# Performance work log

Measured on AMD Instinct MI355X. Metric: run time of the kernel, lower is better.

Reference implementation:

```python
import jax, jax.numpy as jnp
import numpy as np

N_NODES = 100000


def setup_inputs() -> dict:
    key = jax.random.key(0)
    ks = jax.random.split(key, 8)
    N, E, D_IN, D_OUT = N_NODES, 1600000, 64, 64
    return {
        "emb_src": jax.random.normal(ks[0], (N, D_IN), dtype=jnp.float32),
        "emb_dst": jax.random.normal(ks[1], (N, D_IN), dtype=jnp.float32),
        "edge_weight": jax.random.uniform(ks[2], (E,), dtype=jnp.float32),
        "W": jax.random.normal(ks[3], (D_IN, D_OUT), dtype=jnp.float32) / np.sqrt(D_IN),
        "b": jnp.zeros((D_OUT,), dtype=jnp.float32),
        "src_idx": jax.random.randint(ks[4], (E,), 0, N),
        "dst_idx": jax.random.randint(ks[5], (E,), 0, N),
        "user_indices": jax.random.randint(ks[6], (N,), 0, 1000000),
        "labels": jax.random.randint(ks[7], (N,), 0, 2),
        "perm": jnp.arange(N),
    }


def reference(emb_src, emb_dst, edge_weight, W, b, src_idx, dst_idx, user_indices, labels, perm):
    # DGL update_all(u_mul_e('embedding','weight','m'), sum('m','ft')):
    # gather source embeddings, scale by edge weight, scatter-sum into dst.
    msgs = emb_src[src_idx] * edge_weight[:, None]            # [E, D]
    ft = jax.ops.segment_sum(msgs, dst_idx, num_segments=N_NODES)  # [N, D]
    # aggregate == 'SUM': self embedding + aggregated neighborhood
    h = emb_dst + ft                                          # [N, D]
    # per-row np.where(itemlist == dst_ID) matching -> permutation gather
    users = user_indices[perm]
    labs = labels[perm]
    # last layer: tanh(Linear(h)) (dropout p=0 is identity)
    item_embeddings = jnp.tanh(h @ W + b)                     # [N, D_OUT]
    return item_embeddings, users, labs
```

## Files before the change

### kernel.cpp

```cpp
#include <hip/hip_runtime.h>
#include <hip/hip_fp16.h>

#define D 64
#define NQ (D / 4)
#define NB 512
#define NPB 196
#define LOCAL_BITS 8
#define LOCAL_MASK 255
#define SCAN_W 512
#define CAP 4096
#define CAPB 3584

#define HACC_STRIDE 17
#define SMEM_BYTES (D * D * 4 + NPB * HACC_STRIDE * 16)

__device__ __forceinline__ float fast_tanh(float x) {
    float e = __expf(2.0f * x);
    return 1.0f - 2.0f / (e + 1.0f);
}

struct f8 { float4 a, b; };

__global__ __launch_bounds__(512) void init_cursor_kernel(int* __restrict__ cursor)
{
    int t = threadIdx.x;
    if (t < NB) cursor[t] = t * CAPB;
}

__global__ __launch_bounds__(1024) void front_kernel(
    const int* __restrict__ src_idx,
    const int* __restrict__ dst_idx,
    const float* __restrict__ edge_weight,
    int* __restrict__ cursor,
    int2* __restrict__ payload,
    const int* __restrict__ user_indices,
    const int* __restrict__ labels,
    const int* __restrict__ perm,
    const float* __restrict__ emb_src,
    __half* __restrict__ emb_h,
    float* __restrict__ users_out,
    float* __restrict__ labs_out,
    int n_edges, int chunk, int n_nodes)
{
    __shared__ int hist[NB];
    __shared__ int blockbase[NB];
    __shared__ int cur[NB];
    const int tid = threadIdx.x;
    int lo = blockIdx.x * chunk;
    int hi = min(n_edges, lo + chunk);

    for (int i = tid; i < NB; i += 1024) { hist[i] = 0; cur[i] = 0; }
    __syncthreads();
    for (int e = lo + tid; e < hi; e += 1024)
        atomicAdd(&hist[(unsigned)dst_idx[e] / NPB], 1);
    __syncthreads();
    for (int i = tid; i < NB; i += 1024) {
        int c = hist[i];
        blockbase[i] = c ? atomicAdd(&cursor[i], c) : 0;
    }
    __syncthreads();
    for (int e = lo + tid; e < hi; e += 1024) {
        int d = dst_idx[e];
        unsigned bkt = (unsigned)d / NPB;
        int pos = blockbase[bkt] + atomicAdd(&cur[bkt], 1);
        if (pos < (int)(bkt + 1) * CAPB)
            payload[pos] = make_int2((src_idx[e] << LOCAL_BITS) | (d - (int)bkt * NPB),
                                     __float_as_int(edge_weight[e]));
    }

    const int gstride = gridDim.x * blockDim.x;
    const int t0 = blockIdx.x * blockDim.x + tid;
    for (int i = t0; i < n_nodes; i += gstride) {
        int p = perm[i];
        users_out[i] = (float)user_indices[p];
        labs_out[i]  = (float)labels[p];
    }
    const int n_cvt = n_nodes * NQ;
    for (int i = t0; i < n_cvt; i += gstride) {
        float4 v = reinterpret_cast<const float4*>(emb_src)[i];
        __half2 a, b;
        a.x = __float2half_rn(v.x); a.y = __float2half_rn(v.y);
        b.x = __float2half_rn(v.z); b.y = __float2half_rn(v.w);
        uint2 u;
        u.x = *reinterpret_cast<unsigned*>(&a);
        u.y = *reinterpret_cast<unsigned*>(&b);
        reinterpret_cast<uint2*>(emb_h)[i] = u;
    }
}

template <bool USE_H, bool FIXED_BASE>
__global__ __launch_bounds__(1024, 8) void fused_gather_gemm_kernel(
    const float* __restrict__ emb_src,
    const __half* __restrict__ emb_h,
    const float* __restrict__ emb_dst,
    const float* __restrict__ Wmat,
    const float* __restrict__ bias,
    const int2* __restrict__ payload,
    const int* __restrict__ base_or_cursor,
    const int* __restrict__ counts,
    float* __restrict__ out,
    int n_nodes)
{
    __shared__ __align__(16) char smem[SMEM_BYTES];
    float*  Ws     = reinterpret_cast<float*>(smem);
    float4* Hacc   = reinterpret_cast<float4*>(smem + D * D * 4);
    int2*   sedges = reinterpret_cast<int2*>(smem + D * D * 4);
    int*    cnt    = reinterpret_cast<int*>(smem + D * D * 4 + CAP * 8);
    int*    scn    = cnt + 256;
    int*    cur    = scn + 256;

    const int tid = threadIdx.x;
    const int b   = blockIdx.x;
    int start, end;
    if constexpr (FIXED_BASE) {
        start = b * CAPB;
        end   = min(base_or_cursor[b], start + CAPB);
    } else {
        start = base_or_cursor[b];
        end   = start + counts[b];
    }

    const int g8 = tid >> 3;
    const int q8 = tid & 7;
    const float4* esrc = reinterpret_cast<const float4*>(emb_src);

    reinterpret_cast<float4*>(Ws)[tid] = reinterpret_cast<const float4*>(Wmat)[tid];

    auto load_row = [&](unsigned src) -> f8 {
        f8 r;
        if constexpr (USE_H) {
            uint4 u = *reinterpret_cast<const uint4*>(emb_h + ((size_t)src << 6) + (q8 << 3));
            union { uint2 w; __half2 h2[2]; } c0, c1;
            c0.w = make_uint2(u.x, u.y);
            c1.w = make_uint2(u.z, u.w);
            float2 f0 = __half22float2(c0.h2[0]);
            float2 f1 = __half22float2(c0.h2[1]);
            float2 f2 = __half22float2(c1.h2[0]);
            float2 f3 = __half22float2(c1.h2[1]);
            r.a = make_float4(f0.x, f0.y, f1.x, f1.y);
            r.b = make_float4(f2.x, f2.y, f3.x, f3.y);
        } else {
            const float4* p = esrc + (size_t)src * NQ + (q8 << 1);
            r.a = p[0];
            r.b = p[1];
        }
        return r;
    };

    float4 accA[2], accB[2];
    #pragma unroll
    for (int k = 0; k < 2; ++k) {
        accA[k] = make_float4(0.f, 0.f, 0.f, 0.f);
        accB[k] = make_float4(0.f, 0.f, 0.f, 0.f);
    }

    for (int cbase = start; cbase < end; cbase += CAP) {
        const int m = min(end - cbase, CAP);

        for (int i = tid; i < 256; i += 1024) { cnt[i] = 0; cur[i] = 0; }
        __syncthreads();

        int2 pe[4];
        #pragma unroll
        for (int j = 0; j < 4; ++j) {
            int i = cbase + tid + j * 1024;
            if (tid + j * 1024 < m) {
                pe[j] = payload[i];
                atomicAdd(&cnt[pe[j].x & LOCAL_MASK], 1);
            }
        }
        __syncthreads();

        if (tid < 256) scn[tid] = cnt[tid];
        __syncthreads();
        #pragma unroll
        for (int d = 1; d < 256; d <<= 1) {
            int x = 0;
            if (tid < 256 && tid >= d) x = scn[tid - d];
            __syncthreads();
            if (tid < 256) scn[tid] += x;
            __syncthreads();
        }
        if (tid < 256) scn[tid] -= cnt[tid];
        __syncthreads();

        #pragma unroll
        for (int j = 0; j < 4; ++j) {
            if (tid + j * 1024 < m) {
                int local = pe[j].x & LOCAL_MASK;
                int pos = scn[local] + atomicAdd(&cur[local], 1);
                sedges[pos] = pe[j];
            }
        }
        __syncthreads();

        #pragma unroll
        for (int k = 0; k < 2; ++k) {
            int n = g8 + 128 * k;
            if (n < NPB) {
                int mm = cnt[n];
                int bs = scn[n];
                float4 aA = accA[k], aB = accB[k];
                for (int j = 0; j < mm; j += 4) {
                    int lim = mm - 1;
                    int2 e0 = sedges[bs + j];
                    int2 e1 = sedges[bs + min(j + 1, lim)];
                    int2 e2 = sedges[bs + min(j + 2, lim)];
                    int2 e3 = sedges[bs + min(j + 3, lim)];
                    f8 v0 = load_row((unsigned)e0.x >> LOCAL_BITS);
                    f8 v1 = load_row((unsigned)e1.x >> LOCAL_BITS);
                    f8 v2 = load_row((unsigned)e2.x >> LOCAL_BITS);
                    f8 v3 = load_row((unsigned)e3.x >> LOCAL_BITS);
                    float w0 = __int_as_float(e0.y);
                    float w1 = (j + 1 < mm) ? __int_as_float(e1.y) : 0.f;
                    float w2 = (j + 2 < mm) ? __int_as_float(e2.y) : 0.f;
                    float w3 = (j + 3 < mm) ? __int_as_float(e3.y) : 0.f;
                    aA.x += v0.a.x * w0 + v1.a.x * w1 + v2.a.x * w2 + v3.a.x * w3;
                    aA.y += v0.a.y * w0 + v1.a.y * w1 + v2.a.y * w2 + v3.a.y * w3;
                    aA.z += v0.a.z * w0 + v1.a.z * w1 + v2.a.z * w2 + v3.a.z * w3;
                    aA.w += v0.a.w * w0 + v1.a.w * w1 + v2.a.w * w2 + v3.a.w * w3;
                    aB.x += v0.b.x * w0 + v1.b.x * w1 + v2.b.x * w2 + v3.b.x * w3;
                    aB.y += v0.b.y * w0 + v1.b.y * w1 + v2.b.y * w2 + v3.b.y * w3;
                    aB.z += v0.b.z * w0 + v1.b.z * w1 + v2.b.z * w2 + v3.b.z * w3;
                    aB.w += v0.b.w * w0 + v1.b.w * w1 + v2.b.w * w2 + v3.b.w * w3;
                }
                accA[k] = aA; accB[k] = aB;
            }
        }
        __syncthreads();
    }

    const int node0 = b * NPB;
    #pragma unroll
    for (int k = 0; k < 2; ++k) {
        int n = g8 + 128 * k;
        if (n < NPB) {
            int node = node0 + n;
            float4 d0 = make_float4(0.f, 0.f, 0.f, 0.f);
            float4 d1 = make_float4(0.f, 0.f, 0.f, 0.f);
            if (node < n_nodes) {
                const float4* ed = reinterpret_cast<const float4*>(emb_dst)
                                 + (size_t)node * NQ + (q8 << 1);
                d0 = ed[0]; d1 = ed[1];
            }
            float4 aA = accA[k], aB = accB[k];
            aA.x += d0.x; aA.y += d0.y; aA.z += d0.z; aA.w += d0.w;
            aB.x += d1.x; aB.y += d1.y; aB.z += d1.z; aB.w += d1.w;
            Hacc[n * HACC_STRIDE + (q8 << 1)]     = aA;
            Hacc[n * HACC_STRIDE + (q8 << 1) + 1] = aB;
        }
    }
    __syncthreads();

    const int g = tid >> 4;
    const int q = tid & 15;
    const float4* Ws4 = reinterpret_cast<const float4*>(Ws);
    float4 bv = reinterpret_cast<const float4*>(bias)[q];
    #pragma unroll
    for (int k = 0; k < 4; ++k) {
        int n = g + 64 * k;
        int node = node0 + n;
        if (n < NPB && node < n_nodes) {
            float4 a = make_float4(0.f, 0.f, 0.f, 0.f);
            #pragma unroll 4
            for (int kk = 0; kk < 16; ++kk) {
                float4 hv = Hacc[n * HACC_STRIDE + kk];
                float4 w0 = Ws4[(4 * kk + 0) * 16 + q];
                float4 w1 = Ws4[(4 * kk + 1) * 16 + q];
                float4 w2 = Ws4[(4 * kk + 2) * 16 + q];
                float4 w3 = Ws4[(4 * kk + 3) * 16 + q];
                a.x += hv.x * w0.x + hv.y * w1.x + hv.z * w2.x + hv.w * w3.x;
                a.y += hv.x * w0.y + hv.y * w1.y + hv.z * w2.y + hv.w * w3.y;
                a.z += hv.x * w0.z + hv.y * w1.z + hv.z * w2.z + hv.w * w3.z;
                a.w += hv.x * w0.w + hv.y * w1.w + hv.z * w2.w + hv.w * w3.w;
            }
            float4 o;
            o.x = fast_tanh(a.x + bv.x);
            o.y = fast_tanh(a.y + bv.y);
            o.z = fast_tanh(a.z + bv.z);
            o.w = fast_tanh(a.w + bv.w);
            reinterpret_cast<float4*>(out)[(size_t)node * NQ + q] = o;
        }
    }
}

__global__ __launch_bounds__(256) void meta_kernel(
    const int* __restrict__ user_indices,
    const int* __restrict__ labels,
    const int* __restrict__ perm,
    const float* __restrict__ emb_src,
    __half* __restrict__ emb_h,
    float* __restrict__ users_out,
    float* __restrict__ labs_out,
    int* __restrict__ counts,
    int n_zero,
    int n_nodes)
{
    const int stride = gridDim.x * blockDim.x;
    int t0 = blockIdx.x * blockDim.x + threadIdx.x;
    if (counts)
        for (int i = t0; i < n_zero; i += stride) counts[i] = 0;
    for (int i = t0; i < n_nodes; i += stride) {
        int p = perm[i];
        users_out[i] = (float)user_indices[p];
        labs_out[i]  = (float)labels[p];
    }
    if (emb_h) {
        const int n_cvt = n_nodes * NQ;
        for (int i = t0; i < n_cvt; i += stride) {
            float4 v = reinterpret_cast<const float4*>(emb_src)[i];
            __half2 a, b;
            a.x = __float2half_rn(v.x); a.y = __float2half_rn(v.y);
            b.x = __float2half_rn(v.z); b.y = __float2half_rn(v.w);
            uint2 u;
            u.x = *reinterpret_cast<unsigned*>(&a);
            u.y = *reinterpret_cast<unsigned*>(&b);
            reinterpret_cast<uint2*>(emb_h)[i] = u;
        }
    }
}

__global__ __launch_bounds__(1024) void hist_bucket_kernel(
    const int* __restrict__ dst_idx,
    int* __restrict__ counts,
    int n_edges, int chunk)
{
    __shared__ int hist[NB];
    for (int i = threadIdx.x; i < NB; i += 1024) hist[i] = 0;
    __syncthreads();
    int lo = blockIdx.x * chunk;
    int hi = min(n_edges, lo + chunk);
    for (int e = lo + threadIdx.x; e < hi; e += 1024)
        atomicAdd(&hist[(unsigned)dst_idx[e] / NPB], 1);
    __syncthreads();
    for (int i = threadIdx.x; i < NB; i += 1024)
        if (hist[i]) atomicAdd(&counts[i], hist[i]);
}

__global__ __launch_bounds__(SCAN_W) void scan_small_kernel(
    const int* __restrict__ counts,
    int* __restrict__ base,
    int* __restrict__ cursor,
    int nb)
{
    __shared__ int s[SCAN_W];
    int t = threadIdx.x;
    int v = (t < nb) ? counts[t] : 0;
    s[t] = v;
    __syncthreads();
    #pragma unroll
    for (int d = 1; d < SCAN_W; d <<= 1) {
        int x = (t >= d) ? s[t - d] : 0;
        __syncthreads();
        s[t] += x;
        __syncthreads();
    }
    if (t < nb) { base[t] = s[t] - v; cursor[t] = s[t] - v; }
}

__global__ __launch_bounds__(1024) void scatter_bucket_kernel(
    const int* __restrict__ src_idx,
    const int* __restrict__ dst_idx,
    const float* __restrict__ edge_weight,
    int* __restrict__ cursor,
    int2* __restrict__ payload,
    int n_edges, int chunk)
{
    __shared__ int hist[NB];
    __shared__ int blockbase[NB];
    __shared__ int cur[NB];
    const int tid = threadIdx.x;
    int lo = blockIdx.x * chunk;
    int hi = min(n_edges, lo + chunk);

    for (int i = tid; i < NB; i += 1024) { hist[i] = 0; cur[i] = 0; }
    __syncthreads();
    for (int e = lo + tid; e < hi; e += 1024)
        atomicAdd(&hist[(unsigned)dst_idx[e] / NPB], 1);
    __syncthreads();
    for (int i = tid; i < NB; i += 1024) {
        int c = hist[i];
        blockbase[i] = c ? atomicAdd(&cursor[i], c) : 0;
    }
    __syncthreads();
    for (int e = lo + tid; e < hi; e += 1024) {
        int d = dst_idx[e];
        unsigned bkt = (unsigned)d / NPB;
        int pos = blockbase[bkt] + atomicAdd(&cur[bkt], 1);
        payload[pos] = make_int2((src_idx[e] << LOCAL_BITS) | (d - (int)bkt * NPB),
                                 __float_as_int(edge_weight[e]));
    }
}

__global__ __launch_bounds__(256) void init_h_kernel(
    const float* __restrict__ emb_dst, float* __restrict__ h, int n_nodes)
{
    const int stride = gridDim.x * blockDim.x;
    const int total4 = n_nodes * NQ;
    for (int i = blockIdx.x * blockDim.x + threadIdx.x; i < total4; i += stride)
        reinterpret_cast<float4*>(h)[i] = reinterpret_cast<const float4*>(emb_dst)[i];
}

__global__ __launch_bounds__(256) void scatter_kernel(
    const float* __restrict__ emb_src,
    const float* __restrict__ edge_weight,
    const int* __restrict__ src_idx,
    const int* __restrict__ dst_idx,
    float* __restrict__ h,
    int n_edges)
{
    int t = blockIdx.x * blockDim.x + threadIdx.x;
    if (t >= n_edges * NQ) return;
    int e = t >> 4;
    int q = t & 15;
    int s = src_idx[e];
    int d = dst_idx[e];
    float w = edge_weight[e];
    float4 v = reinterpret_cast<const float4*>(emb_src)[(size_t)s * NQ + q];
    float* p = h + (size_t)d * D + q * 4;
    atomicAdd(p + 0, v.x * w);
    atomicAdd(p + 1, v.y * w);
    atomicAdd(p + 2, v.z * w);
    atomicAdd(p + 3, v.w * w);
}

__global__ __launch_bounds__(256, 4) void gemm_tanh_kernel(
    float* __restrict__ h,
    const float* __restrict__ W,
    const float* __restrict__ b,
    int n_nodes)
{
    __shared__ float Ws[D * D];
    __shared__ float Hs[64 * D];

    const int tid = threadIdx.x;

    for (int i = tid; i < D * D / 4; i += 256)
        reinterpret_cast<float4*>(Ws)[i] = reinterpret_cast<const float4*>(W)[i];

    const int tile0 = blockIdx.x * 64;

    for (int i = tid; i < 64 * NQ; i += 256) {
        int row = i >> 4;
        int kq  = i & 15;
        float4 v = make_float4(0.f, 0.f, 0.f, 0.f);
        if (tile0 + row < n_nodes)
            v = reinterpret_cast<const float4*>(h)[(size_t)(tile0 + row) * NQ + kq];
        int kqs = kq ^ ((row >> 2) & 3);
        *reinterpret_cast<float4*>(&Hs[row * D + kqs * 4]) = v;
    }
    __syncthreads();

    const int rbase = (tid >> 4) << 2;
    const int j0    = (tid & 15) << 2;

    float acc[4][4];
    #pragma unroll
    for (int r = 0; r < 4; ++r)
        #pragma unroll
        for (int j = 0; j < 4; ++j) acc[r][j] = 0.f;

    #pragma unroll 4
    for (int kq = 0; kq < 16; ++kq) {
        float4 hv[4];
        #pragma unroll
        for (int r = 0; r < 4; ++r) {
            int row = rbase + r;
            hv[r] = *reinterpret_cast<const float4*>(
                &Hs[row * D + ((kq ^ ((row >> 2) & 3)) << 2)]);
        }
        float4 wv[4];
        #pragma unroll
        for (int kk = 0; kk < 4; ++kk)
            wv[kk] = *reinterpret_cast<const float4*>(&Ws[(kq * 4 + kk) * D + j0]);
        #pragma unroll
        for (int r = 0; r < 4; ++r) {
            acc[r][0] += hv[r].x * wv[0].x + hv[r].y * wv[1].x + hv[r].z * wv[2].x + hv[r].w * wv[3].x;
            acc[r][1] += hv[r].x * wv[0].y + hv[r].y * wv[1].y + hv[r].z * wv[2].y + hv[r].w * wv[3].y;
            acc[r][2] += hv[r].x * wv[0].z + hv[r].y * wv[1].z + hv[r].z * wv[2].z + hv[r].w * wv[3].z;
            acc[r][3] += hv[r].x * wv[0].w + hv[r].y * wv[1].w + hv[r].z * wv[2].w + hv[r].w * wv[3].w;
        }
    }

    float4 bv = *reinterpret_cast<const float4*>(&b[j0]);
    #pragma unroll
    for (int r = 0; r < 4; ++r) {
        int row = tile0 + rbase + r;
        if (row < n_nodes) {
            float4 o;
            o.x = fast_tanh(acc[r][0] + bv.x);
            o.y = fast_tanh(acc[r][1] + bv.y);
            o.z = fast_tanh(acc[r][2] + bv.z);
            o.w = fast_tanh(acc[r][3] + bv.w);
            reinterpret_cast<float4*>(h)[(size_t)row * NQ + (j0 >> 2)] = o;
        }
    }
}

extern "C" void kernel_launch(void* const* d_in, const int* in_sizes, int n_in,
                              void* d_out, int out_size, void* d_ws, size_t ws_size,
                              hipStream_t stream)
{
    const float* emb_src      = (const float*)d_in[0];
    const float* emb_dst      = (const float*)d_in[1];
    const float* edge_weight  = (const float*)d_in[2];
    const float* W            = (const float*)d_in[3];
    const float* b            = (const float*)d_in[4];
    const int*   src_idx      = (const int*)d_in[5];
    const int*   dst_idx      = (const int*)d_in[6];
    const int*   user_indices = (const int*)d_in[7];
    const int*   labels       = (const int*)d_in[8];
    const int*   perm         = (const int*)d_in[9];

    const int n_nodes = in_sizes[7];
    const int n_edges = in_sizes[2];

    float* out       = (float*)d_out;
    float* h         = out;
    float* users_out = out + (size_t)n_nodes * D;
    float* labs_out  = users_out + n_nodes;

    const int nb = (n_nodes + NPB - 1) / NPB;
    const int nblk  = 256;
    const int chunk = (n_edges + nblk - 1) / nblk;

    size_t need_fast = (size_t)NB * 4 + 16 + (size_t)NB * CAPB * 8 + 16
                     + (size_t)n_nodes * D * 2;
    size_t need_sort = (size_t)NB * 4 * 3 + 16 + (size_t)n_edges * 8;
    size_t need_h    = need_sort + 16 + (size_t)n_nodes * D * 2;

    bool shape_ok = (nb <= NB) && (n_nodes <= (1 << (31 - LOCAL_BITS)));
    bool ok_fast  = shape_ok && (ws_size >= need_fast) &&
                    ((size_t)n_edges <= (size_t)NB * CAPB);
    bool ok_sort  = shape_ok && (ws_size >= need_sort);
    bool ok_h     = ok_sort && (ws_size >= need_h);

    if (ok_fast) {
        int*  cursor  = (int*)d_ws;
        int2* payload = (int2*)(((uintptr_t)(cursor + NB) + 15) & ~(uintptr_t)15);
        __half* emb_h = (__half*)(((uintptr_t)(payload + (size_t)NB * CAPB) + 15) & ~(uintptr_t)15);

        init_cursor_kernel<<<1, 512, 0, stream>>>(cursor);
        front_kernel<<<nblk, 1024, 0, stream>>>(
            src_idx, dst_idx, edge_weight, cursor, payload,
            user_indices, labels, perm, emb_src, emb_h,
            users_out, labs_out, n_edges, chunk, n_nodes);
        fused_gather_gemm_kernel<true, true><<<nb, 1024, 0, stream>>>(
            emb_src, emb_h, emb_dst, W, b, payload, cursor, nullptr, out, n_nodes);
    } else if (ok_sort) {
        int*  counts  = (int*)d_ws;
        int*  base    = counts + NB;
        int*  cursor  = base + NB;
        int2* payload = (int2*)(((uintptr_t)(cursor + NB) + 15) & ~(uintptr_t)15);
        __half* emb_h = ok_h ? (__half*)(((uintptr_t)(payload + n_edges) + 15) & ~(uintptr_t)15)
                             : nullptr;

        meta_kernel<<<1024, 256, 0, stream>>>(user_indices, labels, perm,
                                              emb_src, emb_h,
                                              users_out, labs_out, counts, NB, n_nodes);
        hist_bucket_kernel<<<nblk, 1024, 0, stream>>>(dst_idx, counts, n_edges, chunk);
        scan_small_kernel<<<1, SCAN_W, 0, stream>>>(counts, base, cursor, nb);
        scatter_bucket_kernel<<<nblk, 1024, 0, stream>>>(
            src_idx, dst_idx, edge_weight, cursor, payload, n_edges, chunk);
        if (ok_h)
            fused_gather_gemm_kernel<true, false><<<nb, 1024, 0, stream>>>(
                emb_src, emb_h, emb_dst, W, b, payload, base, counts, out, n_nodes);
        else
            fused_gather_gemm_kernel<false, false><<<nb, 1024, 0, stream>>>(
                emb_src, nullptr, emb_dst, W, b, payload, base, counts, out, n_nodes);
    } else {
        meta_kernel<<<512, 256, 0, stream>>>(user_indices, labels, perm,
                                             emb_src, nullptr,
                                             users_out, labs_out, nullptr, 0, n_nodes);
        init_h_kernel<<<2048, 256, 0, stream>>>(emb_dst, h, n_nodes);
        scatter_kernel<<<(n_edges * NQ + 255) / 256, 256, 0, stream>>>(
            emb_src, edge_weight, src_idx, dst_idx, h, n_edges);
        gemm_tanh_kernel<<<(n_nodes + 63) / 64, 256, 0, stream>>>(h, W, b, n_nodes);
    }
}
```

Measured before the change: 81.34 us.

## Split front kernel into scatter and convert blocks; software-prefetch fp16 gather rows

The front kernel now launches extra blocks: the first 256 do the edge bucketing scatter, and the rest handle the perm gather and the fp16 conversion of emb_src. This lets those independent tasks run in parallel instead of serially within each block. The fp16 gather loop in the fused kernel is software-pipelined: the next four edges' rows are loaded before the current four are accumulated, to hide gather latency. This costs more registers, which may lower occupancy, and issues redundant prefetch loads past the end of each node's edge list.

```diff
diff --git a/kernel.cpp b/kernel.cpp
--- a/kernel.cpp
+++ b/kernel.cpp
@@ -10,6 +10,8 @@
 #define SCAN_W 512
 #define CAP 4096
 #define CAPB 3584
+#define SCATTER_BLKS 256
+#define FRONT_BLKS 2048
 
 #define HACC_STRIDE 17
 #define SMEM_BYTES (D * D * 4 + NPB * HACC_STRIDE * 16)
@@ -27,7 +29,7 @@
     if (t < NB) cursor[t] = t * CAPB;
 }
 
-__global__ __launch_bounds__(1024) void front_kernel(
+__global__ __launch_bounds__(1024) void front2_kernel(
     const int* __restrict__ src_idx,
     const int* __restrict__ dst_idx,
     const float* __restrict__ edge_weight,
@@ -42,49 +44,53 @@
     float* __restrict__ labs_out,
     int n_edges, int chunk, int n_nodes)
 {
-    __shared__ int hist[NB];
-    __shared__ int blockbase[NB];
-    __shared__ int cur[NB];
     const int tid = threadIdx.x;
-    int lo = blockIdx.x * chunk;
-    int hi = min(n_edges, lo + chunk);
-
-    for (int i = tid; i < NB; i += 1024) { hist[i] = 0; cur[i] = 0; }
-    __syncthreads();
-    for (int e = lo + tid; e < hi; e += 1024)
-        atomicAdd(&hist[(unsigned)dst_idx[e] / NPB], 1);
-    __syncthreads();
-    for (int i = tid; i < NB; i += 1024) {
-        int c = hist[i];
-        blockbase[i] = c ? atomicAdd(&cursor[i], c) : 0;
-    }
-    __syncthreads();
-    for (int e = lo + tid; e < hi; e += 1024) {
-        int d = dst_idx[e];
-        unsigned bkt = (unsigned)d / NPB;
-        int pos = blockbase[bkt] + atomicAdd(&cur[bkt], 1);
-        if (pos < (int)(bkt + 1) * CAPB)
-            payload[pos] = make_int2((src_idx[e] << LOCAL_BITS) | (d - (int)bkt * NPB),
-                                     __float_as_int(edge_weight[e]));
-    }
-
-    const int gstride = gridDim.x * blockDim.x;
-    const int t0 = blockIdx.x * blockDim.x + tid;
-    for (int i = t0; i < n_nodes; i += gstride) {
-        int p = perm[i];
-        users_out[i] = (float)user_indices[p];
-        labs_out[i]  = (float)labels[p];
-    }
-    const int n_cvt = n_nodes * NQ;
-    for (int i = t0; i < n_cvt; i += gstride) {
-        float4 v = reinterpret_cast<const float4*>(emb_src)[i];
-        __half2 a, b;
-        a.x = __float2half_rn(v.x); a.y = __float2half_rn(v.y);
-        b.x = __float2half_rn(v.z); b.y = __float2half_rn(v.w);
-        uint2 u;
-        u.x = *reinterpret_cast<unsigned*>(&a);
-        u.y = *reinterpret_cast<unsigned*>(&b);
-        reinterpret_cast<uint2*>(emb_h)[i] = u;
+
+    if (blockIdx.x < SCATTER_BLKS) {
+        __shared__ int hist[NB];
+        __shared__ int blockbase[NB];
+        __shared__ int cur[NB];
+        int lo = blockIdx.x * chunk;
+        int hi = min(n_edges, lo + chunk);
+
+        for (int i = tid; i < NB; i += 1024) { hist[i] = 0; cur[i] = 0; }
+        __syncthreads();
+        for (int e = lo + tid; e < hi; e += 1024)
+            atomicAdd(&hist[(unsigned)dst_idx[e] / NPB], 1);
+        __syncthreads();
+        for (int i = tid; i < NB; i += 1024) {
+            int c = hist[i];
+            blockbase[i] = c ? atomicAdd(&cursor[i], c) : 0;
+        }
+        __syncthreads();
+        for (int e = lo + tid; e < hi; e += 1024) {
+            int d = dst_idx[e];
+            unsigned bkt = (unsigned)d / NPB;
+            int pos = blockbase[bkt] + atomicAdd(&cur[bkt], 1);
+            if (pos < (int)(bkt + 1) * CAPB)
+                payload[pos] = make_int2((src_idx[e] << LOCAL_BITS) | (d - (int)bkt * NPB),
+                                         __float_as_int(edge_weight[e]));
+        }
+    } else {
+        const int nblk = gridDim.x - SCATTER_BLKS;
+        const int gstride = nblk * 1024;
+        const int t0 = (blockIdx.x - SCATTER_BLKS) * 1024 + tid;
+        for (int i = t0; i < n_nodes; i += gstride) {
+            int p = perm[i];
+            users_out[i] = (float)user_indices[p];
+            labs_out[i]  = (float)labels[p];
+        }
+        const int n_cvt = n_nodes * NQ;
+        for (int i = t0; i < n_cvt; i += gstride) {
+            float4 v = reinterpret_cast<const float4*>(emb_src)[i];
+            __half2 a, b;
+            a.x = __float2half_rn(v.x); a.y = __float2half_rn(v.y);
+            b.x = __float2half_rn(v.z); b.y = __float2half_rn(v.w);
+            uint2 u;
+            u.x = *reinterpret_cast<unsigned*>(&a);
+            u.y = *reinterpret_cast<unsigned*>(&b);
+            reinterpret_cast<uint2*>(emb_h)[i] = u;
+        }
     }
 }
 
@@ -126,27 +132,6 @@
 
     reinterpret_cast<float4*>(Ws)[tid] = reinterpret_cast<const float4*>(Wmat)[tid];
 
-    auto load_row = [&](unsigned src) -> f8 {
-        f8 r;
-        if constexpr (USE_H) {
-            uint4 u = *reinterpret_cast<const uint4*>(emb_h + ((size_t)src << 6) + (q8 << 3));
-            union { uint2 w; __half2 h2[2]; } c0, c1;
-            c0.w = make_uint2(u.x, u.y);
-            c1.w = make_uint2(u.z, u.w);
-            float2 f0 = __half22float2(c0.h2[0]);
-            float2 f1 = __half22float2(c0.h2[1]);
-            float2 f2 = __half22float2(c1.h2[0]);
-            float2 f3 = __half22float2(c1.h2[1]);
-            r.a = make_float4(f0.x, f0.y, f1.x, f1.y);
-            r.b = make_float4(f2.x, f2.y, f3.x, f3.y);
-        } else {
-            const float4* p = esrc + (size_t)src * NQ + (q8 << 1);
-            r.a = p[0];
-            r.b = p[1];
-        }
-        return r;
-    };
-
     float4 accA[2], accB[2];
     #pragma unroll
     for (int k = 0; k < 2; ++k) {
@@ -200,29 +185,90 @@
             if (n < NPB) {
                 int mm = cnt[n];
                 int bs = scn[n];
+                if (mm <= 0) continue;
+                int lim = mm - 1;
                 float4 aA = accA[k], aB = accB[k];
-                for (int j = 0; j < mm; j += 4) {
-                    int lim = mm - 1;
-                    int2 e0 = sedges[bs + j];
-                    int2 e1 = sedges[bs + min(j + 1, lim)];
-                    int2 e2 = sedges[bs + min(j + 2, lim)];
-                    int2 e3 = sedges[bs + min(j + 3, lim)];
-                    f8 v0 = load_row((unsigned)e0.x >> LOCAL_BITS);
-                    f8 v1 = load_row((unsigned)e1.x >> LOCAL_BITS);
-                    f8 v2 = load_row((unsigned)e2.x >> LOCAL_BITS);
-                    f8 v3 = load_row((unsigned)e3.x >> LOCAL_BITS);
-                    float w0 = __int_as_float(e0.y);
-                    float w1 = (j + 1 < mm) ? __int_as_float(e1.y) : 0.f;
-                    float w2 = (j + 2 < mm) ? __int_as_float(e2.y) : 0.f;
-                    float w3 = (j + 3 < mm) ? __int_as_float(e3.y) : 0.f;
-                    aA.x += v0.a.x * w0 + v1.a.x * w1 + v2.a.x * w2 + v3.a.x * w3;
-                    aA.y += v0.a.y * w0 + v1.a.y * w1 + v2.a.y * w2 + v3.a.y * w3;
-                    aA.z += v0.a.z * w0 + v1.a.z * w1 + v2.a.z * w2 + v3.a.z * w3;
-                    aA.w += v0.a.w * w0 + v1.a.w * w1 + v2.a.w * w2 + v3.a.w * w3;
-                    aB.x += v0.b.x * w0 + v1.b.x * w1 + v2.b.x * w2 + v3.b.x * w3;
-                    aB.y += v0.b.y * w0 + v1.b.y * w1 + v2.b.y * w2 + v3.b.y * w3;
-                    aB.z += v0.b.z * w0 + v1.b.z * w1 + v2.b.z * w2 + v3.b.z * w3;
-                    aB.w += v0.b.w * w0 + v1.b.w * w1 + v2.b.w * w2 + v3.b.w * w3;
+
+                if constexpr (USE_H) {
+                    int2 e0 = sedges[bs];
+                    int2 e1 = sedges[bs + min(1, lim)];
+                    int2 e2 = sedges[bs + min(2, lim)];
+                    int2 e3 = sedges[bs + min(3, lim)];
+                    uint4 u0 = *reinterpret_cast<const uint4*>(
+                        emb_h + ((size_t)((unsigned)e0.x >> LOCAL_BITS) << 6) + (q8 << 3));
+                    uint4 u1 = *reinterpret_cast<const uint4*>(
+                        emb_h + ((size_t)((unsigned)e1.x >> LOCAL_BITS) << 6) + (q8 << 3));
+                    uint4 u2 = *reinterpret_cast<const uint4*>(
+                        emb_h + ((size_t)((unsigned)e2.x >> LOCAL_BITS) << 6) + (q8 << 3));
+                    uint4 u3 = *reinterpret_cast<const uint4*>(
+                        emb_h + ((size_t)((unsigned)e3.x >> LOCAL_BITS) << 6) + (q8 << 3));
+
+                    for (int j = 0; j < mm; j += 4) {
+                        int jn = j + 4;
+                        int2 f0 = sedges[bs + min(jn,     lim)];
+                        int2 f1 = sedges[bs + min(jn + 1, lim)];
+                        int2 f2 = sedges[bs + min(jn + 2, lim)];
+                        int2 f3 = sedges[bs + min(jn + 3, lim)];
+                        uint4 w0v = *reinterpret_cast<const uint4*>(
+                            emb_h + ((size_t)((unsigned)f0.x >> LOCAL_BITS) << 6) + (q8 << 3));
+                        uint4 w1v = *reinterpret_cast<const uint4*>(
+                            emb_h + ((size_t)((unsigned)f1.x >> LOCAL_BITS) << 6) + (q8 << 3));
+                        uint4 w2v = *reinterpret_cast<const uint4*>(
+                            emb_h + ((size_t)((unsigned)f2.x >> LOCAL_BITS) << 6) + (q8 << 3));
+                        uint4 w3v = *reinterpret_cast<const uint4*>(
+                            emb_h + ((size_t)((unsigned)f3.x >> LOCAL_BITS) << 6) + (q8 << 3));
+
+                        float w0 = __int_as_float(e0.y);
+                        float w1 = (j + 1 < mm) ? __int_as_float(e1.y) : 0.f;
+                        float w2 = (j + 2 < mm) ? __int_as_float(e2.y) : 0.f;
+                        float w3 = (j + 3 < mm) ? __int_as_float(e3.y) : 0.f;
+                        {
+                            union { uint4 u; __half2 h2[4]; } c0{u0}, c1{u1}, c2{u2}, c3{u3};
+                            float2 p00 = __half22float2(c0.h2[0]), p01 = __half22float2(c0.h2[1]);
+                            float2 p02 = __half22float2(c0.h2[2]), p03 = __half22float2(c0.h2[3]);
+                            float2 p10 = __half22float2(c1.h2[0]), p11 = __half22float2(c1.h2[1]);
+                            float2 p12 = __half22float2(c1.h2[2]), p13 = __half22float2(c1.h2[3]);
+                            float2 p20 = __half22float2(c2.h2[0]), p21 = __half22float2(c2.h2[1]);
+                            float2 p22 = __half22float2(c2.h2[2]), p23 = __half22float2(c2.h2[3]);
+                            float2 p30 = __half22float2(c3.h2[0]), p31 = __half22float2(c3.h2[1]);
+                            float2 p32 = __half22float2(c3.h2[2]), p33 = __half22float2(c3.h2[3]);
+                            aA.x += p00.x * w0 + p10.x * w1 + p20.x * w2 + p30.x * w3;
+                            aA.y += p00.y * w0 + p10.y * w1 + p20.y * w2 + p30.y * w3;
+                            aA.z += p01.x * w0 + p11.x * w1 + p21.x * w2 + p31.x * w3;
+                            aA.w += p01.y * w0 + p11.y * w1 + p21.y * w2 + p31.y * w3;
+                            aB.x += p02.x * w0 + p12.x * w1 + p22.x * w2 + p32.x * w3;
+                            aB.y += p02.y * w0 + p12.y * w1 + p22.y * w2 + p32.y * w3;
+                            aB.z += p03.x * w0 + p13.x * w1 + p23.x * w2 + p33.x * w3;
+                            aB.w += p03.y * w0 + p13.y * w1 + p23.y * w2 + p33.y * w3;
+                        }
+                        e0 = f0; e1 = f1; e2 = f2; e3 = f3;
+                        u0 = w0v; u1 = w1v; u2 = w2v; u3 = w3v;
+                    }
+                } else {
+                    for (int j = 0; j < mm; j += 4) {
+                        int2 e0 = sedges[bs + j];
+                        int2 e1 = sedges[bs + min(j + 1, lim)];
+                        int2 e2 = sedges[bs + min(j + 2, lim)];
+                        int2 e3 = sedges[bs + min(j + 3, lim)];
+                        const float4* p0 = esrc + (size_t)((unsigned)e0.x >> LOCAL_BITS) * NQ + (q8 << 1);
+                        const float4* p1 = esrc + (size_t)((unsigned)e1.x >> LOCAL_BITS) * NQ + (q8 << 1);
+                        const float4* p2 = esrc + (size_t)((unsigned)e2.x >> LOCAL_BITS) * NQ + (q8 << 1);
+                        const float4* p3 = esrc + (size_t)((unsigned)e3.x >> LOCAL_BITS) * NQ + (q8 << 1);
+                        float4 a0 = p0[0], b0 = p0[1], a1 = p1[0], b1 = p1[1];
+                        float4 a2 = p2[0], b2 = p2[1], a3 = p3[0], b3 = p3[1];
+                        float w0 = __int_as_float(e0.y);
+                        float w1 = (j + 1 < mm) ? __int_as_float(e1.y) : 0.f;
+                        float w2 = (j + 2 < mm) ? __int_as_float(e2.y) : 0.f;
+                        float w3 = (j + 3 < mm) ? __int_as_float(e3.y) : 0.f;
+                        aA.x += a0.x * w0 + a1.x * w1 + a2.x * w2 + a3.x * w3;
+                        aA.y += a0.y * w0 + a1.y * w1 + a2.y * w2 + a3.y * w3;
+                        aA.z += a0.z * w0 + a1.z * w1 + a2.z * w2 + a3.z * w3;
+                        aA.w += a0.w * w0 + a1.w * w1 + a2.w * w2 + a3.w * w3;
+                        aB.x += b0.x * w0 + b1.x * w1 + b2.x * w2 + b3.x * w3;
+                        aB.y += b0.y * w0 + b1.y * w1 + b2.y * w2 + b3.y * w3;
+                        aB.z += b0.z * w0 + b1.z * w1 + b2.z * w2 + b3.z * w3;
+                        aB.w += b0.w * w0 + b1.w * w1 + b2.w * w2 + b3.w * w3;
+                    }
                 }
                 accA[k] = aA; accB[k] = aB;
             }
@@ -521,8 +567,7 @@
     float* labs_out  = users_out + n_nodes;
 
     const int nb = (n_nodes + NPB - 1) / NPB;
-    const int nblk  = 256;
-    const int chunk = (n_edges + nblk - 1) / nblk;
+    const int chunk = (n_edges + SCATTER_BLKS - 1) / SCATTER_BLKS;
 
     size_t need_fast = (size_t)NB * 4 + 16 + (size_t)NB * CAPB * 8 + 16
                      + (size_t)n_nodes * D * 2;
@@ -541,7 +586,7 @@
         __half* emb_h = (__half*)(((uintptr_t)(payload + (size_t)NB * CAPB) + 15) & ~(uintptr_t)15);
 
         init_cursor_kernel<<<1, 512, 0, stream>>>(cursor);
-        front_kernel<<<nblk, 1024, 0, stream>>>(
+        front2_kernel<<<FRONT_BLKS, 1024, 0, stream>>>(
             src_idx, dst_idx, edge_weight, cursor, payload,
             user_indices, labels, perm, emb_src, emb_h,
             users_out, labs_out, n_edges, chunk, n_nodes);
@@ -554,14 +599,15 @@
         int2* payload = (int2*)(((uintptr_t)(cursor + NB) + 15) & ~(uintptr_t)15);
         __half* emb_h = ok_h ? (__half*)(((uintptr_t)(payload + n_edges) + 15) & ~(uintptr_t)15)
                              : nullptr;
+        const int chunk2 = (n_edges + 255) / 256;
 
         meta_kernel<<<1024, 256, 0, stream>>>(user_indices, labels, perm,
                                               emb_src, emb_h,
                                               users_out, labs_out, counts, NB, n_nodes);
-        hist_bucket_kernel<<<nblk, 1024, 0, stream>>>(dst_idx, counts, n_edges, chunk);
+        hist_bucket_kernel<<<256, 1024, 0, stream>>>(dst_idx, counts, n_edges, chunk2);
         scan_small_kernel<<<1, SCAN_W, 0, stream>>>(counts, base, cursor, nb);
-        scatter_bucket_kernel<<<nblk, 1024, 0, stream>>>(
-            src_idx, dst_idx, edge_weight, cursor, payload, n_edges, chunk);
+        scatter_bucket_kernel<<<256, 1024, 0, stream>>>(
+            src_idx, dst_idx, edge_weight, cursor, payload, n_edges, chunk2);
         if (ok_h)
             fused_gather_gemm_kernel<true, false><<<nb, 1024, 0, stream>>>(
                 emb_src, emb_h, emb_dst, W, b, payload, base, counts, out, n_nodes);
```

Measured after the change: 80.68 us. Within noise of the previous version (-0.8%).

## Split front kernel into scatter and conversion block roles; use wave-shuffle scan

Applied to the files above, without the earlier changes.

The front kernel now launches 2048 blocks. The first 256 keep the edge bucketing and scatter, and the remaining blocks handle the perm gather and the fp16 conversion of emb_src, so that memory-bound conversion work runs alongside the scatter instead of after it on the same threads. In the gather kernel, the 256-entry shared-memory Hillis-Steele scan, which used about 16 barriers, is replaced by a wave-level __shfl_up scan plus a small cross-wave combine. The extra front blocks add launch and scheduling overhead and may compete with the scatter blocks for bandwidth.

```diff
diff --git a/kernel.cpp b/kernel.cpp
--- a/kernel.cpp
+++ b/kernel.cpp
@@ -10,6 +10,8 @@
 #define SCAN_W 512
 #define CAP 4096
 #define CAPB 3584
+#define SCATTER_BLKS 256
+#define FRONT_BLKS 2048
 
 #define HACC_STRIDE 17
 #define SMEM_BYTES (D * D * 4 + NPB * HACC_STRIDE * 16)
@@ -27,7 +29,7 @@
     if (t < NB) cursor[t] = t * CAPB;
 }
 
-__global__ __launch_bounds__(1024) void front_kernel(
+__global__ __launch_bounds__(1024) void front2_kernel(
     const int* __restrict__ src_idx,
     const int* __restrict__ dst_idx,
     const float* __restrict__ edge_weight,
@@ -42,49 +44,53 @@
     float* __restrict__ labs_out,
     int n_edges, int chunk, int n_nodes)
 {
-    __shared__ int hist[NB];
-    __shared__ int blockbase[NB];
-    __shared__ int cur[NB];
     const int tid = threadIdx.x;
-    int lo = blockIdx.x * chunk;
-    int hi = min(n_edges, lo + chunk);
-
-    for (int i = tid; i < NB; i += 1024) { hist[i] = 0; cur[i] = 0; }
-    __syncthreads();
-    for (int e = lo + tid; e < hi; e += 1024)
-        atomicAdd(&hist[(unsigned)dst_idx[e] / NPB], 1);
-    __syncthreads();
-    for (int i = tid; i < NB; i += 1024) {
-        int c = hist[i];
-        blockbase[i] = c ? atomicAdd(&cursor[i], c) : 0;
-    }
-    __syncthreads();
-    for (int e = lo + tid; e < hi; e += 1024) {
-        int d = dst_idx[e];
-        unsigned bkt = (unsigned)d / NPB;
-        int pos = blockbase[bkt] + atomicAdd(&cur[bkt], 1);
-        if (pos < (int)(bkt + 1) * CAPB)
-            payload[pos] = make_int2((src_idx[e] << LOCAL_BITS) | (d - (int)bkt * NPB),
-                                     __float_as_int(edge_weight[e]));
-    }
-
-    const int gstride = gridDim.x * blockDim.x;
-    const int t0 = blockIdx.x * blockDim.x + tid;
-    for (int i = t0; i < n_nodes; i += gstride) {
-        int p = perm[i];
-        users_out[i] = (float)user_indices[p];
-        labs_out[i]  = (float)labels[p];
-    }
-    const int n_cvt = n_nodes * NQ;
-    for (int i = t0; i < n_cvt; i += gstride) {
-        float4 v = reinterpret_cast<const float4*>(emb_src)[i];
-        __half2 a, b;
-        a.x = __float2half_rn(v.x); a.y = __float2half_rn(v.y);
-        b.x = __float2half_rn(v.z); b.y = __float2half_rn(v.w);
-        uint2 u;
-        u.x = *reinterpret_cast<unsigned*>(&a);
-        u.y = *reinterpret_cast<unsigned*>(&b);
-        reinterpret_cast<uint2*>(emb_h)[i] = u;
+
+    if (blockIdx.x < SCATTER_BLKS) {
+        __shared__ int hist[NB];
+        __shared__ int blockbase[NB];
+        __shared__ int cur[NB];
+        int lo = blockIdx.x * chunk;
+        int hi = min(n_edges, lo + chunk);
+
+        for (int i = tid; i < NB; i += 1024) { hist[i] = 0; cur[i] = 0; }
+        __syncthreads();
+        for (int e = lo + tid; e < hi; e += 1024)
+            atomicAdd(&hist[(unsigned)dst_idx[e] / NPB], 1);
+        __syncthreads();
+        for (int i = tid; i < NB; i += 1024) {
+            int c = hist[i];
+            blockbase[i] = c ? atomicAdd(&cursor[i], c) : 0;
+        }
+        __syncthreads();
+        for (int e = lo + tid; e < hi; e += 1024) {
+            int d = dst_idx[e];
+            unsigned bkt = (unsigned)d / NPB;
+            int pos = blockbase[bkt] + atomicAdd(&cur[bkt], 1);
+            if (pos < (int)(bkt + 1) * CAPB)
+                payload[pos] = make_int2((src_idx[e] << LOCAL_BITS) | (d - (int)bkt * NPB),
+                                         __float_as_int(edge_weight[e]));
+        }
+    } else {
+        const int nblk = gridDim.x - SCATTER_BLKS;
+        const int gstride = nblk * 1024;
+        const int t0 = (blockIdx.x - SCATTER_BLKS) * 1024 + tid;
+        for (int i = t0; i < n_nodes; i += gstride) {
+            int p = perm[i];
+            users_out[i] = (float)user_indices[p];
+            labs_out[i]  = (float)labels[p];
+        }
+        const int n_cvt = n_nodes * NQ;
+        for (int i = t0; i < n_cvt; i += gstride) {
+            float4 v = reinterpret_cast<const float4*>(emb_src)[i];
+            __half2 a, b;
+            a.x = __float2half_rn(v.x); a.y = __float2half_rn(v.y);
+            b.x = __float2half_rn(v.z); b.y = __float2half_rn(v.w);
+            uint2 u;
+            u.x = *reinterpret_cast<unsigned*>(&a);
+            u.y = *reinterpret_cast<unsigned*>(&b);
+            reinterpret_cast<uint2*>(emb_h)[i] = u;
+        }
     }
 }
 
@@ -108,6 +114,7 @@
     int*    cnt    = reinterpret_cast<int*>(smem + D * D * 4 + CAP * 8);
     int*    scn    = cnt + 256;
     int*    cur    = scn + 256;
+    int*    wsum   = cur + 256;
 
     const int tid = threadIdx.x;
     const int b   = blockIdx.x;
@@ -171,18 +178,27 @@
         }
         __syncthreads();
 
-        if (tid < 256) scn[tid] = cnt[tid];
-        __syncthreads();
-        #pragma unroll
-        for (int d = 1; d < 256; d <<= 1) {
-            int x = 0;
-            if (tid < 256 && tid >= d) x = scn[tid - d];
+        {
+            int v = 0;
+            if (tid < 256) v = cnt[tid];
+            int x = v;
+            #pragma unroll
+            for (int d = 1; d < 64; d <<= 1) {
+                int y = __shfl_up(x, d, 64);
+                if ((tid & 63) >= d) x += y;
+            }
+            if (tid < 256 && (tid & 63) == 63) wsum[tid >> 6] = x;
             __syncthreads();
-            if (tid < 256) scn[tid] += x;
+            if (tid < 256) {
+                int w = tid >> 6;
+                int off = 0;
+                if (w > 0) off += wsum[0];
+                if (w > 1) off += wsum[1];
+                if (w > 2) off += wsum[2];
+                scn[tid] = x + off - v;
+            }
             __syncthreads();
         }
-        if (tid < 256) scn[tid] -= cnt[tid];
-        __syncthreads();
 
         #pragma unroll
         for (int j = 0; j < 4; ++j) {
@@ -521,8 +537,7 @@
     float* labs_out  = users_out + n_nodes;
 
     const int nb = (n_nodes + NPB - 1) / NPB;
-    const int nblk  = 256;
-    const int chunk = (n_edges + nblk - 1) / nblk;
+    const int chunk = (n_edges + SCATTER_BLKS - 1) / SCATTER_BLKS;
 
     size_t need_fast = (size_t)NB * 4 + 16 + (size_t)NB * CAPB * 8 + 16
                      + (size_t)n_nodes * D * 2;
@@ -541,7 +556,7 @@
         __half* emb_h = (__half*)(((uintptr_t)(payload + (size_t)NB * CAPB) + 15) & ~(uintptr_t)15);
 
         init_cursor_kernel<<<1, 512, 0, stream>>>(cursor);
-        front_kernel<<<nblk, 1024, 0, stream>>>(
+        front2_kernel<<<FRONT_BLKS, 1024, 0, stream>>>(
             src_idx, dst_idx, edge_weight, cursor, payload,
             user_indices, labels, perm, emb_src, emb_h,
             users_out, labs_out, n_edges, chunk, n_nodes);
@@ -554,14 +569,15 @@
         int2* payload = (int2*)(((uintptr_t)(cursor + NB) + 15) & ~(uintptr_t)15);
         __half* emb_h = ok_h ? (__half*)(((uintptr_t)(payload + n_edges) + 15) & ~(uintptr_t)15)
                              : nullptr;
+        const int chunk2 = (n_edges + 255) / 256;
 
         meta_kernel<<<1024, 256, 0, stream>>>(user_indices, labels, perm,
                                               emb_src, emb_h,
                                               users_out, labs_out, counts, NB, n_nodes);
-        hist_bucket_kernel<<<nblk, 1024, 0, stream>>>(dst_idx, counts, n_edges, chunk);
+        hist_bucket_kernel<<<256, 1024, 0, stream>>>(dst_idx, counts, n_edges, chunk2);
         scan_small_kernel<<<1, SCAN_W, 0, stream>>>(counts, base, cursor, nb);
-        scatter_bucket_kernel<<<nblk, 1024, 0, stream>>>(
-            src_idx, dst_idx, edge_weight, cursor, payload, n_edges, chunk);
+        scatter_bucket_kernel<<<256, 1024, 0, stream>>>(
+            src_idx, dst_idx, edge_weight, cursor, payload, n_edges, chunk2);
         if (ok_h)
             fused_gather_gemm_kernel<true, false><<<nb, 1024, 0, stream>>>(
                 emb_src, emb_h, emb_dst, W, b, payload, base, counts, out, n_nodes);
```

Measured after the change: 83.07 us. 1.02x slower.
